# Optimization experiments

Measured on AMD Instinct MI355X. Metric: run time of the kernel, lower is better.

Reference implementation:

```python
import jax, jax.numpy as jnp
import numpy as np

N = 100000   # nodes
F = 32       # input features
E = 1600000  # edges
G = 512      # graphs
EPS = 1e-5   # BatchNorm eps


def setup_inputs() -> dict:
    key = jax.random.key(0)
    ks = jax.random.split(key, 12)
    x = jax.random.normal(ks[0], (N, F), jnp.float32)
    edge_index = jax.random.randint(ks[1], (2, E), 0, N)
    batch = jnp.sort(jax.random.randint(ks[2], (N,), 0, G))

    def glorot(k, i, o):
        return jax.random.normal(k, (i, o), jnp.float32) * (1.0 / np.sqrt(i))

    return {
        "x": x, "edge_index": edge_index, "batch": batch,
        "W1": glorot(ks[3], F, 16), "b1": jnp.zeros((16,), jnp.float32),
        "g1": jnp.ones((16,), jnp.float32), "be1": jnp.zeros((16,), jnp.float32),
        "W2": glorot(ks[4], 16, 64), "b2": jnp.zeros((64,), jnp.float32),
        "g2": jnp.ones((64,), jnp.float32), "be2": jnp.zeros((64,), jnp.float32),
        "W3": glorot(ks[5], 64, 64), "b3": jnp.zeros((64,), jnp.float32),
        "Wc": glorot(ks[6], 64, 1), "bc": jnp.zeros((1,), jnp.float32),
    }


def _gcn_conv(h, src, dst, dis, W, b, n):
    # PyG GCNConv: D^{-1/2}(A+I)D^{-1/2} X W + b (self-loops folded in analytically)
    hw = h @ W                                   # [N, out]
    msg = hw[src] * (dis[src] * dis[dst])[:, None]   # gather + normalize, [E, out]
    agg = jax.ops.segment_sum(msg, dst, num_segments=n)  # scatter-add
    agg = agg + hw * (dis * dis)[:, None]        # self-loop contribution
    return agg + b


def _bn(h, g, b):
    # BatchNorm1d, training mode (biased variance over node axis)
    m = jnp.mean(h, axis=0)
    v = jnp.mean((h - m) ** 2, axis=0)
    return (h - m) * jax.lax.rsqrt(v + EPS) * g + b


def reference(x, edge_index, batch, W1, b1, g1, be1, W2, b2, g2, be2, W3, b3, Wc, bc):
    n = x.shape[0]
    src, dst = edge_index[0], edge_index[1]
    # degree including self-loops (computed on target nodes, edge weight 1)
    deg = jax.ops.segment_sum(jnp.ones((src.shape[0],), x.dtype), dst, num_segments=n) + 1.0
    dis = jax.lax.rsqrt(deg)

    h = jnp.tanh(_gcn_conv(x, src, dst, dis, W1, b1, n))
    h = _bn(h, g1, be1)
    h = jnp.tanh(_gcn_conv(h, src, dst, dis, W2, b2, n))
    h = _bn(h, g2, be2)
    h = jnp.tanh(_gcn_conv(h, src, dst, dis, W3, b3, n))

    # global_mean_pool over graph ids
    sums = jax.ops.segment_sum(h, batch, num_segments=G)          # [G, 64]
    cnts = jax.ops.segment_sum(jnp.ones((n,), x.dtype), batch, num_segments=G)
    pooled = sums / jnp.maximum(cnts, 1.0)[:, None]

    return pooled @ Wc + bc   # [G, 1]
```

## Files before the change

kernel.cpp:

```cpp
#include <hip/hip_runtime.h>

#define EPSV 1e-5f
#define EB 512
#define NPB 256
#define NBUK_MAX 512
#define FCAP 12288

typedef __attribute__((ext_vector_type(8))) short bf16x8;
typedef __attribute__((ext_vector_type(4))) float f32x4;
typedef unsigned short ushort_t;

__device__ inline unsigned f2bf(float f){
  unsigned u = __float_as_uint(f);
  u += 0x7fffu + ((u>>16)&1u);
  return u>>16;
}
#define BF_LO(u) __uint_as_float((u)<<16)
#define BF_HI(u) __uint_as_float((u)&0xffff0000u)

__global__ __launch_bounds__(256) void k_csr_count(const int* __restrict__ dst, int E, int chunk,
                                                   int nbuk, int* __restrict__ cnt){
  __shared__ int hist[NBUK_MAX];
  int t = threadIdx.x, b = blockIdx.x;
  for(int k=t; k<nbuk; k+=256) hist[k]=0;
  __syncthreads();
  int lo = b*chunk, hi = lo+chunk < E ? lo+chunk : E;
  for(int i=lo+t*4; i+3<hi; i+=1024){
    int4 d4 = *(const int4*)(dst + i);
    atomicAdd(&hist[d4.x>>8], 1); atomicAdd(&hist[d4.y>>8], 1);
    atomicAdd(&hist[d4.z>>8], 1); atomicAdd(&hist[d4.w>>8], 1);
  }
  int rem = lo + ((hi - lo) & ~3);
  for(int i=rem+t; i<hi; i+=256) atomicAdd(&hist[dst[i]>>8], 1);
  __syncthreads();
  for(int k=t; k<nbuk; k+=256) cnt[(size_t)k*EB + b] = hist[k];
}

__global__ __launch_bounds__(1024) void k_scan_local(const int* __restrict__ v_in, int L,
                                                     int* __restrict__ loc, int* __restrict__ blk){
  __shared__ int ps[1024];
  int t = threadIdx.x;
  int i = blockIdx.x*1024 + t;
  int v = (i < L) ? v_in[i] : 0;
  ps[t] = v;
  __syncthreads();
  for(int off=1; off<1024; off<<=1){
    int u = (t>=off) ? ps[t-off] : 0;
    __syncthreads();
    ps[t] += u;
    __syncthreads();
  }
  if(i < L) loc[i] = ps[t] - v;
  if(t == 1023) blk[blockIdx.x] = ps[t];
}

__global__ __launch_bounds__(1024) void k_scan_sums(int* __restrict__ blk, int nb,
                                                    int* __restrict__ totalOut){
  __shared__ int ps[1024];
  int t = threadIdx.x;
  int v = (t < nb) ? blk[t] : 0;
  ps[t] = v;
  __syncthreads();
  for(int off=1; off<1024; off<<=1){
    int u = (t>=off) ? ps[t-off] : 0;
    __syncthreads();
    ps[t] += u;
    __syncthreads();
  }
  if(t < nb) blk[t] = ps[t] - v;
  if(t == 1023) *totalOut = ps[t];
}

__global__ __launch_bounds__(256) void k_csr_scatter(const int* __restrict__ src,
                                                     const int* __restrict__ dst,
                                                     const int* __restrict__ loc,
                                                     const int* __restrict__ blk,
                                                     int E, int chunk, int nbuk,
                                                     unsigned* __restrict__ epk){
  __shared__ int cur[NBUK_MAX];
  int t = threadIdx.x, b = blockIdx.x;
  for(int k=t; k<nbuk; k+=256){
    int i = k*EB + b;
    cur[k] = loc[i] + blk[i>>10];
  }
  __syncthreads();
  int lo = b*chunk, hi = lo+chunk < E ? lo+chunk : E;
  for(int i=lo+t*4; i+3<hi; i+=1024){
    int4 s4 = *(const int4*)(src + i);
    int4 d4 = *(const int4*)(dst + i);
    int p0 = atomicAdd(&cur[d4.x>>8], 1);
    epk[p0] = ((unsigned)s4.x<<8) | (unsigned)(d4.x & 255);
    int p1 = atomicAdd(&cur[d4.y>>8], 1);
    epk[p1] = ((unsigned)s4.y<<8) | (unsigned)(d4.y & 255);
    int p2 = atomicAdd(&cur[d4.z>>8], 1);
    epk[p2] = ((unsigned)s4.z<<8) | (unsigned)(d4.z & 255);
    int p3 = atomicAdd(&cur[d4.w>>8], 1);
    epk[p3] = ((unsigned)s4.w<<8) | (unsigned)(d4.w & 255);
  }
  int rem = lo + ((hi - lo) & ~3);
  for(int i=rem+t; i<hi; i+=256){
    int d = dst[i];
    int p = atomicAdd(&cur[d>>8], 1);
    epk[p] = ((unsigned)src[i]<<8) | (unsigned)(d & 255);
  }
}

__global__ __launch_bounds__(256) void k_csr_final(const unsigned* __restrict__ epk,
                                                   const int* __restrict__ loc,
                                                   const int* __restrict__ blk,
                                                   int nbuk, int N, int E,
                                                   int* __restrict__ rp, float* __restrict__ dis,
                                                   int* __restrict__ csr_src){
  __shared__ int hist[NPB], ps[NPB], cur[NPB];
  __shared__ unsigned eld[FCAP];
  int t = threadIdx.x, k = blockIdx.x;
  int i0 = k*EB;
  int base = loc[i0] + blk[i0>>10];
  int next;
  if(k+1 < nbuk){ int i1 = (k+1)*EB; next = loc[i1] + blk[i1>>10]; }
  else next = E;
  int cntk = next - base;
  int node0 = k*NPB;
  bool inLds = (cntk <= FCAP);
  hist[t] = 0;
  __syncthreads();
  if(inLds){
    for(int i=t; i<cntk; i+=256){
      unsigned e = epk[base+i];
      eld[i] = e;
      atomicAdd(&hist[(int)(e & 255u)], 1);
    }
  } else {
    for(int i=t; i<cntk; i+=256) atomicAdd(&hist[(int)(epk[base+i] & 255u)], 1);
  }
  __syncthreads();
  int deg = hist[t];
  ps[t] = deg;
  __syncthreads();
  for(int off=1; off<256; off<<=1){
    int u = (t>=off) ? ps[t-off] : 0;
    __syncthreads();
    ps[t] += u;
    __syncthreads();
  }
  int lb = ps[t] - deg;
  int n = node0 + t;
  if(n < N){
    rp[n]  = base + lb;
    dis[n] = rsqrtf((float)deg + 1.0f);
  }
  cur[t] = base + lb;
  __syncthreads();
  if(inLds){
    for(int i=t; i<cntk; i+=256){
      unsigned e = eld[i];
      int p = atomicAdd(&cur[(int)(e & 255u)], 1);
      csr_src[p] = (int)(e >> 8);
    }
  } else {
    for(int i=t; i<cntk; i+=256){
      unsigned e = epk[base+i];
      int p = atomicAdd(&cur[(int)(e & 255u)], 1);
      csr_src[p] = (int)(e >> 8);
    }
  }
  if(k == nbuk-1 && t == 0) rp[N] = E;
}

__global__ __launch_bounds__(256) void k_gemm1(const float* __restrict__ x,
                                               const float* __restrict__ W,
                                               const float* __restrict__ dis,
                                               int N, ushort_t* __restrict__ P1){
  __shared__ __align__(16) float Ws[32*16];
  int t = threadIdx.x;
  for(int i=t; i<32*16; i+=256) Ws[i] = W[i];
  __syncthreads();
  int row = blockIdx.x*256 + t;
  if(row >= N) return;
  const float4* xr = (const float4*)(x + (size_t)row*32);
  float acc[16];
  #pragma unroll
  for(int j=0;j<16;j++) acc[j]=0.f;
  #pragma unroll
  for(int k4=0;k4<8;k4++){
    float4 v = xr[k4];
    float vv[4] = {v.x, v.y, v.z, v.w};
    #pragma unroll
    for(int kk=0;kk<4;kk++){
      float h = vv[kk];
      const float* wr = &Ws[(k4*4+kk)*16];
      #pragma unroll
      for(int j=0;j<16;j++) acc[j] += h*wr[j];
    }
  }
  float d = dis[row];
  unsigned q[8];
  #pragma unroll
  for(int j=0;j<8;j++)
    q[j] = f2bf(acc[2*j]*d) | (f2bf(acc[2*j+1]*d)<<16);
  uint4* o = (uint4*)(P1 + (size_t)row*16);
  o[0] = make_uint4(q[0],q[1],q[2],q[3]);
  o[1] = make_uint4(q[4],q[5],q[6],q[7]);
}

__global__ __launch_bounds__(256) void k_gather1(const int* __restrict__ rp,
    const int* __restrict__ csr_src,
    const float* __restrict__ dis, const ushort_t* __restrict__ P1,
    const float* __restrict__ bias, int N, ushort_t* __restrict__ Q1,
    float* __restrict__ sdis, float* __restrict__ partials){
  int t = threadIdx.x;
  int idx = blockIdx.x*256 + t;
  int n = idx >> 1, g = t & 1;
  float v[8];
  #pragma unroll
  for(int j=0;j<8;j++) v[j]=0.f;

  if(n < N){
    int beg = rp[n], end = rp[n+1];
    const uint4* Pv = (const uint4*)P1;
    uint4 u = Pv[(size_t)n*2 + g];
    float a0 = BF_LO(u.x), a1 = BF_HI(u.x), a2 = BF_LO(u.y), a3 = BF_HI(u.y);
    float a4 = BF_LO(u.z), a5 = BF_HI(u.z), a6 = BF_LO(u.w), a7 = BF_HI(u.w);
    float b0=0.f,b1=0.f,b2=0.f,b3=0.f,b4=0.f,b5=0.f,b6=0.f,b7=0.f;
    float sd = 0.f;
    int j = beg;
    for(; j+3 < end; j += 4){
      int s0 = csr_src[j], s1 = csr_src[j+1], s2 = csr_src[j+2], s3 = csr_src[j+3];
      uint4 u0 = Pv[(size_t)s0*2 + g];
      uint4 u1 = Pv[(size_t)s1*2 + g];
      uint4 u2 = Pv[(size_t)s2*2 + g];
      uint4 u3 = Pv[(size_t)s3*2 + g];
      if(g==0) sd += (dis[s0] + dis[s1]) + (dis[s2] + dis[s3]);
      a0 += BF_LO(u0.x); a1 += BF_HI(u0.x); a2 += BF_LO(u0.y); a3 += BF_HI(u0.y);
      a4 += BF_LO(u0.z); a5 += BF_HI(u0.z); a6 += BF_LO(u0.w); a7 += BF_HI(u0.w);
      b0 += BF_LO(u1.x); b1 += BF_HI(u1.x); b2 += BF_LO(u1.y); b3 += BF_HI(u1.y);
      b4 += BF_LO(u1.z); b5 += BF_HI(u1.z); b6 += BF_LO(u1.w); b7 += BF_HI(u1.w);
      a0 += BF_LO(u2.x); a1 += BF_HI(u2.x); a2 += BF_LO(u2.y); a3 += BF_HI(u2.y);
      a4 += BF_LO(u2.z); a5 += BF_HI(u2.z); a6 += BF_LO(u2.w); a7 += BF_HI(u2.w);
      b0 += BF_LO(u3.x); b1 += BF_HI(u3.x); b2 += BF_LO(u3.y); b3 += BF_HI(u3.y);
      b4 += BF_LO(u3.z); b5 += BF_HI(u3.z); b6 += BF_LO(u3.w); b7 += BF_HI(u3.w);
    }
    for(; j < end; ++j){
      int s0 = csr_src[j];
      uint4 u0 = Pv[(size_t)s0*2 + g];
      if(g==0) sd += dis[s0];
      a0 += BF_LO(u0.x); a1 += BF_HI(u0.x); a2 += BF_LO(u0.y); a3 += BF_HI(u0.y);
      a4 += BF_LO(u0.z); a5 += BF_HI(u0.z); a6 += BF_LO(u0.w); a7 += BF_HI(u0.w);
    }
    float d = dis[n];
    float4 bb0 = *(const float4*)(bias + g*8);
    float4 bb1 = *(const float4*)(bias + g*8 + 4);
    v[0] = tanhf((a0+b0)*d + bb0.x); v[1] = tanhf((a1+b1)*d + bb0.y);
    v[2] = tanhf((a2+b2)*d + bb0.z); v[3] = tanhf((a3+b3)*d + bb0.w);
    v[4] = tanhf((a4+b4)*d + bb1.x); v[5] = tanhf((a5+b5)*d + bb1.y);
    v[6] = tanhf((a6+b6)*d + bb1.z); v[7] = tanhf((a7+b7)*d + bb1.w);
    uint4 o;
    o.x = f2bf(v[0]*d) | (f2bf(v[1]*d)<<16);
    o.y = f2bf(v[2]*d) | (f2bf(v[3]*d)<<16);
    o.z = f2bf(v[4]*d) | (f2bf(v[5]*d)<<16);
    o.w = f2bf(v[6]*d) | (f2bf(v[7]*d)<<16);
    *(uint4*)(Q1 + (size_t)n*16 + g*8) = o;
    if(g==0) sdis[n] = sd;
  }

  int lane = t & 63, wid = t >> 6;
  __shared__ float redS[4][2][8], redQ[4][2][8];
  #pragma unroll
  for(int j=0;j<8;j++){
    float s = v[j], q = v[j]*v[j];
    #pragma unroll
    for(int off=32; off>=2; off>>=1){
      s += __shfl_down(s, off, 64);
      q += __shfl_down(q, off, 64);
    }
    if(lane < 2){ redS[wid][lane][j] = s; redQ[wid][lane][j] = q; }
  }
  __syncthreads();
  if(t < 16){
    int gg = t>>3, j = t&7;
    float S = redS[0][gg][j]+redS[1][gg][j]+redS[2][gg][j]+redS[3][gg][j];
    float Q = redQ[0][gg][j]+redQ[1][gg][j]+redQ[2][gg][j]+redQ[3][gg][j];
    partials[(size_t)blockIdx.x*32 + t]      = S;
    partials[(size_t)blockIdx.x*32 + 16 + t] = Q;
  }
}

template<int C>
__global__ __launch_bounds__(256) void k_bn_red(const float* __restrict__ partials, int nblk,
                                                float* __restrict__ red){
  constexpr int W = 2*C;
  constexpr int RPF = 256/W;
  int t = threadIdx.x;
  int c = t % W, r0 = t / W;
  float acc = 0.f;
  for(int r = blockIdx.x*RPF + r0; r < nblk; r += 64*RPF)
    acc += partials[(size_t)r*W + c];
  __shared__ float ls[256];
  ls[t] = acc;
  __syncthreads();
  if(t < W){
    float s = 0.f;
    #pragma unroll
    for(int k=0;k<RPF;k++) s += ls[k*W + t];
    red[blockIdx.x*W + t] = s;
  }
}

__global__ __launch_bounds__(256) void k_bn_finprep2b(const float* __restrict__ red,
                           const float* __restrict__ gw, const float* __restrict__ be,
                           float invN, const float* __restrict__ W,
                           ushort_t* __restrict__ wf, float* __restrict__ cp){
  __shared__ float s0[16], s1[16], scf[16], shf[16];
  int t = threadIdx.x;
  if(t < 32){
    float s = 0.f;
    for(int r=0;r<64;r++) s += red[r*32 + t];
    if(t < 16) s0[t] = s; else s1[t-16] = s;
  }
  __syncthreads();
  if(t < 16){
    float m = s0[t]*invN;
    float var = fmaxf(s1[t]*invN - m*m, 0.f);
    float inv = rsqrtf(var + EPSV);
    float sc = gw[t]*inv;
    scf[t] = sc;
    shf[t] = be[t] - m*sc;
  }
  __syncthreads();
  int total = 4*64*8;
  for(int idx=t; idx<total; idx+=256){
    int e = idx & 7;
    int l = (idx>>3) & 63;
    int ct = idx>>9;
    int k = (l>>4)*8 + e;
    int col = ct*16 + (l&15);
    float v = (k < 16) ? scf[k]*W[k*64 + col] : 0.f;
    wf[idx] = (ushort_t)f2bf(v);
  }
  if(t < 64){
    float s = 0.f;
    for(int k=0;k<16;k++) s += shf[k]*W[k*64 + t];
    cp[t] = s;
  }
}

__global__ __launch_bounds__(256) void k_bn_finprep3(const float* __restrict__ red,
                           const float* __restrict__ gw, const float* __restrict__ be,
                           float invN, const float* __restrict__ W,
                           ushort_t* __restrict__ wf, float* __restrict__ cp){
  __shared__ float s0[64], s1[64], scf[64], shf[64];
  int t = threadIdx.x;
  if(t < 128){
    float s = 0.f;
    for(int r=0;r<64;r++) s += red[r*128 + t];
    if(t < 64) s0[t] = s; else s1[t-64] = s;
  }
  __syncthreads();
  if(t < 64){
    float m = s0[t]*invN;
    float var = fmaxf(s1[t]*invN - m*m, 0.f);
    float inv = rsqrtf(var + EPSV);
    float sc = gw[t]*inv;
    scf[t] = sc;
    shf[t] = be[t] - m*sc;
  }
  __syncthreads();
  int total = 4*2*64*8;
  for(int idx=t; idx<total; idx+=256){
    int e = idx & 7;
    int l = (idx>>3) & 63;
    int slot = idx>>9;
    int ct = slot>>1, half = slot&1;
    int k = (l>>4)*8 + e + half*32;
    int col = ct*16 + (l&15);
    wf[idx] = (ushort_t)f2bf(scf[k]*W[k*64 + col]);
  }
  if(t < 64){
    float s = 0.f;
    for(int k=0;k<64;k++) s += shf[k]*W[k*64 + t];
    cp[t] = s;
  }
}

__global__ __launch_bounds__(256) void k_gather2(const int* __restrict__ rp,
    const int* __restrict__ csr_src, const ushort_t* __restrict__ Q1,
    int N, ushort_t* __restrict__ M2){
  int t = threadIdx.x;
  int idx = blockIdx.x*256 + t;
  int n = idx >> 1, g = t & 1;
  if(n >= N) return;
  int beg = rp[n], end = rp[n+1];
  const uint4* Pv = (const uint4*)Q1;
  uint4 u = Pv[(size_t)n*2 + g];
  float a0 = BF_LO(u.x), a1 = BF_HI(u.x), a2 = BF_LO(u.y), a3 = BF_HI(u.y);
  float a4 = BF_LO(u.z), a5 = BF_HI(u.z), a6 = BF_LO(u.w), a7 = BF_HI(u.w);
  float b0=0.f,b1=0.f,b2=0.f,b3=0.f,b4=0.f,b5=0.f,b6=0.f,b7=0.f;
  int j = beg;
  for(; j+3 < end; j += 4){
    int s0 = csr_src[j], s1 = csr_src[j+1], s2 = csr_src[j+2], s3 = csr_src[j+3];
    uint4 u0 = Pv[(size_t)s0*2 + g];
    uint4 u1 = Pv[(size_t)s1*2 + g];
    uint4 u2 = Pv[(size_t)s2*2 + g];
    uint4 u3 = Pv[(size_t)s3*2 + g];
    a0 += BF_LO(u0.x); a1 += BF_HI(u0.x); a2 += BF_LO(u0.y); a3 += BF_HI(u0.y);
    a4 += BF_LO(u0.z); a5 += BF_HI(u0.z); a6 += BF_LO(u0.w); a7 += BF_HI(u0.w);
    b0 += BF_LO(u1.x); b1 += BF_HI(u1.x); b2 += BF_LO(u1.y); b3 += BF_HI(u1.y);
    b4 += BF_LO(u1.z); b5 += BF_HI(u1.z); b6 += BF_LO(u1.w); b7 += BF_HI(u1.w);
    a0 += BF_LO(u2.x); a1 += BF_HI(u2.x); a2 += BF_LO(u2.y); a3 += BF_HI(u2.y);
    a4 += BF_LO(u2.z); a5 += BF_HI(u2.z); a6 += BF_LO(u2.w); a7 += BF_HI(u2.w);
    b0 += BF_LO(u3.x); b1 += BF_HI(u3.x); b2 += BF_LO(u3.y); b3 += BF_HI(u3.y);
    b4 += BF_LO(u3.z); b5 += BF_HI(u3.z); b6 += BF_LO(u3.w); b7 += BF_HI(u3.w);
  }
  for(; j < end; ++j){
    int s0 = csr_src[j];
    uint4 u0 = Pv[(size_t)s0*2 + g];
    a0 += BF_LO(u0.x); a1 += BF_HI(u0.x); a2 += BF_LO(u0.y); a3 += BF_HI(u0.y);
    a4 += BF_LO(u0.z); a5 += BF_HI(u0.z); a6 += BF_LO(u0.w); a7 += BF_HI(u0.w);
  }
  uint4 o;
  o.x = f2bf(a0+b0) | (f2bf(a1+b1)<<16);
  o.y = f2bf(a2+b2) | (f2bf(a3+b3)<<16);
  o.z = f2bf(a4+b4) | (f2bf(a5+b5)<<16);
  o.w = f2bf(a6+b6) | (f2bf(a7+b7)<<16);
  *(uint4*)(M2 + (size_t)n*16 + g*8) = o;
}

__global__ __launch_bounds__(256) void k_mfma2(const ushort_t* __restrict__ M2,
                                               const ushort_t* __restrict__ wf,
                                               const float* __restrict__ cp,
                                               const float* __restrict__ dis,
                                               const float* __restrict__ sdis,
                                               const float* __restrict__ b2,
                                               int N, ushort_t* __restrict__ Q2,
                                               float* __restrict__ partials){
  int t = threadIdx.x, wid = t>>6, l = t&63;
  int r0 = blockIdx.x*128 + wid*32;

  bf16x8 bfr[4];
  #pragma unroll
  for(int ct=0; ct<4; ct++)
    bfr[ct] = *(const bf16x8*)(wf + ((size_t)ct*64 + l)*8);

  bf16x8 af[2];
  #pragma unroll
  for(int rt=0; rt<2; rt++){
    int arow = r0 + rt*16 + (l&15);
    int k0 = (l>>4)*8;
    if(arow < N && k0 < 16) af[rt] = *(const bf16x8*)(M2 + (size_t)arow*16 + k0);
    else                    af[rt] = (bf16x8){0,0,0,0,0,0,0,0};
  }

  f32x4 acc[2][4];
  #pragma unroll
  for(int rt=0; rt<2; rt++)
    #pragma unroll
    for(int ct=0; ct<4; ct++)
      acc[rt][ct] = (f32x4){0.f,0.f,0.f,0.f};

  #pragma unroll
  for(int rt=0; rt<2; rt++)
    #pragma unroll
    for(int ct=0; ct<4; ct++)
      acc[rt][ct] = __builtin_amdgcn_mfma_f32_16x16x32_bf16(af[rt], bfr[ct], acc[rt][ct], 0, 0, 0);

  float cpc[4], blc[4];
  #pragma unroll
  for(int ct=0; ct<4; ct++){
    int col = ct*16 + (l&15);
    cpc[ct] = cp[col]; blc[ct] = b2[col];
  }

  float S4[4] = {0.f,0.f,0.f,0.f}, Q4[4] = {0.f,0.f,0.f,0.f};
  #pragma unroll
  for(int rt=0; rt<2; rt++){
    int rbase = r0 + rt*16 + (l>>4)*4;
    #pragma unroll
    for(int reg=0; reg<4; reg++){
      int row = rbase + reg;
      if(row < N){
        float d = dis[row];
        float sg = sdis[row] + d;
        #pragma unroll
        for(int ct=0; ct<4; ct++){
          float h = tanhf(d*(acc[rt][ct][reg] + sg*cpc[ct]) + blc[ct]);
          Q2[(size_t)row*64 + ct*16 + (l&15)] = (ushort_t)f2bf(h*d);
          S4[ct] += h; Q4[ct] += h*h;
        }
      }
    }
  }
  #pragma unroll
  for(int ct=0; ct<4; ct++){
    S4[ct] += __shfl_xor(S4[ct], 16, 64);
    S4[ct] += __shfl_xor(S4[ct], 32, 64);
    Q4[ct] += __shfl_xor(Q4[ct], 16, 64);
    Q4[ct] += __shfl_xor(Q4[ct], 32, 64);
  }
  __shared__ float wsm[4][64], wqm[4][64];
  if(l < 16){
    #pragma unroll
    for(int ct=0; ct<4; ct++){
      wsm[wid][ct*16 + l] = S4[ct];
      wqm[wid][ct*16 + l] = Q4[ct];
    }
  }
  __syncthreads();
  if(t < 64){
    float S = wsm[0][t]+wsm[1][t]+wsm[2][t]+wsm[3][t];
    float Q = wqm[0][t]+wqm[1][t]+wqm[2][t]+wqm[3][t];
    partials[(size_t)blockIdx.x*128 + t]      = S;
    partials[(size_t)blockIdx.x*128 + 64 + t] = Q;
  }
}

__global__ __launch_bounds__(256) void k_gather3(const int* __restrict__ rp,
    const int* __restrict__ csr_src, const ushort_t* __restrict__ Q2,
    int N, ushort_t* __restrict__ M3){
  int t = threadIdx.x;
  int idx = blockIdx.x*256 + t;
  int n = idx >> 3, g = t & 7;
  if(n >= N) return;
  int beg = rp[n], end = rp[n+1];
  const uint4* Pv = (const uint4*)Q2;
  uint4 u = Pv[(size_t)n*8 + g];
  float a0 = BF_LO(u.x), a1 = BF_HI(u.x), a2 = BF_LO(u.y), a3 = BF_HI(u.y);
  float a4 = BF_LO(u.z), a5 = BF_HI(u.z), a6 = BF_LO(u.w), a7 = BF_HI(u.w);
  float b0=0.f,b1=0.f,b2=0.f,b3=0.f,b4=0.f,b5=0.f,b6=0.f,b7=0.f;
  int j = beg;
  for(; j+3 < end; j += 4){
    int s0 = csr_src[j], s1 = csr_src[j+1], s2 = csr_src[j+2], s3 = csr_src[j+3];
    uint4 u0 = Pv[(size_t)s0*8 + g];
    uint4 u1 = Pv[(size_t)s1*8 + g];
    uint4 u2 = Pv[(size_t)s2*8 + g];
    uint4 u3 = Pv[(size_t)s3*8 + g];
    a0 += BF_LO(u0.x); a1 += BF_HI(u0.x); a2 += BF_LO(u0.y); a3 += BF_HI(u0.y);
    a4 += BF_LO(u0.z); a5 += BF_HI(u0.z); a6 += BF_LO(u0.w); a7 += BF_HI(u0.w);
    b0 += BF_LO(u1.x); b1 += BF_HI(u1.x); b2 += BF_LO(u1.y); b3 += BF_HI(u1.y);
    b4 += BF_LO(u1.z); b5 += BF_HI(u1.z); b6 += BF_LO(u1.w); b7 += BF_HI(u1.w);
    a0 += BF_LO(u2.x); a1 += BF_HI(u2.x); a2 += BF_LO(u2.y); a3 += BF_HI(u2.y);
    a4 += BF_LO(u2.z); a5 += BF_HI(u2.z); a6 += BF_LO(u2.w); a7 += BF_HI(u2.w);
    b0 += BF_LO(u3.x); b1 += BF_HI(u3.x); b2 += BF_LO(u3.y); b3 += BF_HI(u3.y);
    b4 += BF_LO(u3.z); b5 += BF_HI(u3.z); b6 += BF_LO(u3.w); b7 += BF_HI(u3.w);
  }
  for(; j < end; ++j){
    int s0 = csr_src[j];
    uint4 u0 = Pv[(size_t)s0*8 + g];
    a0 += BF_LO(u0.x); a1 += BF_HI(u0.x); a2 += BF_LO(u0.y); a3 += BF_HI(u0.y);
    a4 += BF_LO(u0.z); a5 += BF_HI(u0.z); a6 += BF_LO(u0.w); a7 += BF_HI(u0.w);
  }
  uint4 o;
  o.x = f2bf(a0+b0) | (f2bf(a1+b1)<<16);
  o.y = f2bf(a2+b2) | (f2bf(a3+b3)<<16);
  o.z = f2bf(a4+b4) | (f2bf(a5+b5)<<16);
  o.w = f2bf(a6+b6) | (f2bf(a7+b7)<<16);
  *(uint4*)(M3 + (size_t)n*8*8 + g*8) = o;
}

__global__ __launch_bounds__(256) void k_mfma_head(const ushort_t* __restrict__ M3,
                                                   const ushort_t* __restrict__ wf,
                                                   const float* __restrict__ cp,
                                                   const float* __restrict__ dis,
                                                   const float* __restrict__ sdis,
                                                   const float* __restrict__ b3,
                                                   const float* __restrict__ Wc,
                                                   int N, float* __restrict__ y){
  int t = threadIdx.x, wid = t>>6, l = t&63;
  int r0 = blockIdx.x*128 + wid*32;

  bf16x8 bfr[4][2];
  #pragma unroll
  for(int ct=0; ct<4; ct++)
    #pragma unroll
    for(int h=0; h<2; h++)
      bfr[ct][h] = *(const bf16x8*)(wf + ((size_t)(ct*2+h)*64 + l)*8);

  bf16x8 af[2][2];
  #pragma unroll
  for(int rt=0; rt<2; rt++){
    int arow = r0 + rt*16 + (l&15);
    int k0 = (l>>4)*8;
    #pragma unroll
    for(int h=0; h<2; h++){
      if(arow < N) af[rt][h] = *(const bf16x8*)(M3 + (size_t)arow*64 + k0 + h*32);
      else         af[rt][h] = (bf16x8){0,0,0,0,0,0,0,0};
    }
  }

  f32x4 acc[2][4];
  #pragma unroll
  for(int rt=0; rt<2; rt++)
    #pragma unroll
    for(int ct=0; ct<4; ct++)
      acc[rt][ct] = (f32x4){0.f,0.f,0.f,0.f};

  #pragma unroll
  for(int rt=0; rt<2; rt++)
    #pragma unroll
    for(int ct=0; ct<4; ct++)
      #pragma unroll
      for(int h=0; h<2; h++)
        acc[rt][ct] = __builtin_amdgcn_mfma_f32_16x16x32_bf16(af[rt][h], bfr[ct][h], acc[rt][ct], 0, 0, 0);

  float cpc[4], blc[4], wcc[4];
  #pragma unroll
  for(int ct=0; ct<4; ct++){
    int col = ct*16 + (l&15);
    cpc[ct] = cp[col]; blc[ct] = b3[col]; wcc[ct] = Wc[col];
  }

  #pragma unroll
  for(int rt=0; rt<2; rt++){
    int rbase = r0 + rt*16 + (l>>4)*4;
    #pragma unroll
    for(int reg=0; reg<4; reg++){
      int row = rbase + reg;
      bool ok = (row < N);
      float d  = ok ? dis[row] : 0.f;
      float sg = ok ? (sdis[row] + d) : 0.f;
      float s = 0.f;
      #pragma unroll
      for(int ct=0; ct<4; ct++){
        float h = tanhf(d*(acc[rt][ct][reg] + sg*cpc[ct]) + blc[ct]);
        s += h*wcc[ct];
      }
      s += __shfl_xor(s, 1, 64);
      s += __shfl_xor(s, 2, 64);
      s += __shfl_xor(s, 4, 64);
      s += __shfl_xor(s, 8, 64);
      if(ok && (l&15)==0) y[row] = s;
    }
  }
}

__global__ __launch_bounds__(64) void k_pool2(const float* __restrict__ y,
                                              const int* __restrict__ batch, int N,
                                              const float* __restrict__ bc,
                                              float* __restrict__ out){
  int gId = blockIdx.x;
  int t = threadIdx.x;
  int lo=0, hi=N;
  while(lo<hi){ int mid=(lo+hi)>>1; if(batch[mid] < gId) lo=mid+1; else hi=mid; }
  int start = lo;
  lo=start; hi=N;
  while(lo<hi){ int mid=(lo+hi)>>1; if(batch[mid] < gId+1) lo=mid+1; else hi=mid; }
  int end = lo;

  float s = 0.f;
  for(int r = start+t; r < end; r += 64) s += y[r];
  #pragma unroll
  for(int o=32; o>0; o>>=1) s += __shfl_down(s, o, 64);
  if(t == 0){
    float cnt = (float)(end - start);
    out[gId] = s / fmaxf(cnt, 1.0f) + bc[0];
  }
}

extern "C" void kernel_launch(void* const* d_in, const int* in_sizes, int n_in,
                              void* d_out, int out_size, void* d_ws, size_t ws_size,
                              hipStream_t stream) {
  const float* x     = (const float*)d_in[0];
  const int*   ei    = (const int*)d_in[1];
  const int*   batch = (const int*)d_in[2];
  const float* W1 = (const float*)d_in[3];
  const float* b1 = (const float*)d_in[4];
  const float* g1 = (const float*)d_in[5];
  const float* be1= (const float*)d_in[6];
  const float* W2 = (const float*)d_in[7];
  const float* b2 = (const float*)d_in[8];
  const float* g2 = (const float*)d_in[9];
  const float* be2= (const float*)d_in[10];
  const float* W3 = (const float*)d_in[11];
  const float* b3 = (const float*)d_in[12];
  const float* Wc = (const float*)d_in[13];
  const float* bc = (const float*)d_in[14];

  int N = in_sizes[2];
  int E = in_sizes[1] / 2;
  int G = out_size;
  const int* srcp = ei;
  const int* dstp = ei + E;
  float* out = (float*)d_out;

  auto cdiv = [](long long a, long long b){ return (int)((a+b-1)/b); };
  auto al16 = [](size_t s){ return (s + 15) & ~(size_t)15; };
  int nbuk  = cdiv(N, NPB);
  int chunk = 4*cdiv(E, (long long)EB*4);
  int L     = nbuk * EB;
  int nbL   = cdiv(L, 1024);
  int nblk16 = cdiv((long long)N*2, 256);
  int nblk64 = cdiv((long long)N*8, 256);
  int nblkM  = cdiv(N, 128);

  char* w = (char*)d_ws;
  ushort_t* Q1       = (ushort_t*)w; w += al16((size_t)N*16*2);
  ushort_t* P1       = (ushort_t*)w; w += al16((size_t)N*16*2);
  ushort_t* M2       = (ushort_t*)w; w += al16((size_t)N*16*2);
  ushort_t* Q2       = (ushort_t*)w; w += al16((size_t)N*64*2);
  ushort_t* M3       = (ushort_t*)w; w += al16((size_t)N*64*2);
  float*    dis      = (float*)w;    w += al16((size_t)N*4);
  float*    sdis     = (float*)w;    w += al16((size_t)N*4);
  float*    yv       = (float*)w;    w += al16((size_t)N*4);
  int*      row_ptr  = (int*)w;      w += al16((size_t)(N+1)*4);
  int*      csr_src  = (int*)w;      w += al16((size_t)E*4);
  unsigned* epk      = (unsigned*)w; w += al16((size_t)E*4);
  int*      cnt      = (int*)w;      w += al16((size_t)L*4);
  int*      scan_loc = (int*)w;      w += al16((size_t)L*4);
  int*      scan_blk = (int*)w;      w += al16(1024*4);
  float*    partials = (float*)w;    w += al16((size_t)nblk64*128*4);
  float*    red      = (float*)w;    w += al16(64*128*4);
  float*    cp       = (float*)w;    w += al16(64*4);
  ushort_t* wf       = (ushort_t*)w; w += al16(8*64*8*2);

  k_csr_count<<<EB,256,0,stream>>>(dstp, E, chunk, nbuk, cnt);
  k_scan_local<<<nbL,1024,0,stream>>>(cnt, L, scan_loc, scan_blk);
  k_scan_sums<<<1,1024,0,stream>>>(scan_blk, nbL, row_ptr + N);
  k_csr_scatter<<<EB,256,0,stream>>>(srcp, dstp, scan_loc, scan_blk, E, chunk, nbuk, epk);
  k_csr_final<<<nbuk,256,0,stream>>>(epk, scan_loc, scan_blk, nbuk, N, E, row_ptr, dis, csr_src);

  k_gemm1<<<cdiv(N,256),256,0,stream>>>(x, W1, dis, N, P1);
  k_gather1<<<nblk16,256,0,stream>>>(row_ptr, csr_src, dis, P1, b1, N, Q1, sdis, partials);
  k_bn_red<16><<<64,256,0,stream>>>(partials, nblk16, red);
  k_bn_finprep2b<<<1,256,0,stream>>>(red, g1, be1, 1.0f/N, W2, wf, cp);

  k_gather2<<<nblk16,256,0,stream>>>(row_ptr, csr_src, Q1, N, M2);
  k_mfma2<<<nblkM,256,0,stream>>>(M2, wf, cp, dis, sdis, b2, N, Q2, partials);
  k_bn_red<64><<<64,256,0,stream>>>(partials, nblkM, red);
  k_bn_finprep3<<<1,256,0,stream>>>(red, g2, be2, 1.0f/N, W3, wf, cp);

  k_gather3<<<nblk64,256,0,stream>>>(row_ptr, csr_src, Q2, N, M3);
  k_mfma_head<<<cdiv(N,128),256,0,stream>>>(M3, wf, cp, dis, sdis, b3, Wc, N, yv);

  k_pool2<<<G,64,0,stream>>>(yv, batch, N, bc, out);
}
```

Before: 176.6 us.

## Fuse CSR build and BN reduction stages into cooperative kernels with grid sync

```diff
diff --git a/kernel.cpp b/kernel.cpp
--- a/kernel.cpp
+++ b/kernel.cpp
@@ -1,4 +1,6 @@
 #include <hip/hip_runtime.h>
+#include <hip/hip_cooperative_groups.h>
+namespace cg = cooperative_groups;
 
 #define EPSV 1e-5f
 #define EB 512
@@ -18,153 +20,140 @@
 #define BF_LO(u) __uint_as_float((u)<<16)
 #define BF_HI(u) __uint_as_float((u)&0xffff0000u)
 
-__global__ __launch_bounds__(256) void k_csr_count(const int* __restrict__ dst, int E, int chunk,
-                                                   int nbuk, int* __restrict__ cnt){
-  __shared__ int hist[NBUK_MAX];
+__global__ __launch_bounds__(256) void k_csr_coop(const int* __restrict__ src,
+    const int* __restrict__ dst, int E, int chunk, int nbuk,
+    int* __restrict__ cnt, int* __restrict__ posloc, int* __restrict__ btot,
+    int* __restrict__ bbase, unsigned* __restrict__ epk,
+    int N, int* __restrict__ rp, float* __restrict__ dis, int* __restrict__ csr_src){
+  cg::grid_group grid = cg::this_grid();
+  __shared__ int sA[FCAP];
+  __shared__ int sB[256], sC[256], sD[256];
   int t = threadIdx.x, b = blockIdx.x;
-  for(int k=t; k<nbuk; k+=256) hist[k]=0;
+  int lo = b*chunk, hi = lo+chunk < E ? lo+chunk : E;
+
+  for(int k=t; k<nbuk; k+=256) sA[k]=0;
   __syncthreads();
-  int lo = b*chunk, hi = lo+chunk < E ? lo+chunk : E;
   for(int i=lo+t*4; i+3<hi; i+=1024){
     int4 d4 = *(const int4*)(dst + i);
-    atomicAdd(&hist[d4.x>>8], 1); atomicAdd(&hist[d4.y>>8], 1);
-    atomicAdd(&hist[d4.z>>8], 1); atomicAdd(&hist[d4.w>>8], 1);
-  }
-  int rem = lo + ((hi - lo) & ~3);
-  for(int i=rem+t; i<hi; i+=256) atomicAdd(&hist[dst[i]>>8], 1);
+    atomicAdd(&sA[d4.x>>8],1); atomicAdd(&sA[d4.y>>8],1);
+    atomicAdd(&sA[d4.z>>8],1); atomicAdd(&sA[d4.w>>8],1);
+  }
+  {
+    int rem = lo + ((hi - lo) & ~3);
+    for(int i=rem+t; i<hi; i+=256) atomicAdd(&sA[dst[i]>>8],1);
+  }
   __syncthreads();
-  for(int k=t; k<nbuk; k+=256) cnt[(size_t)k*EB + b] = hist[k];
-}
-
-__global__ __launch_bounds__(1024) void k_scan_local(const int* __restrict__ v_in, int L,
-                                                     int* __restrict__ loc, int* __restrict__ blk){
-  __shared__ int ps[1024];
-  int t = threadIdx.x;
-  int i = blockIdx.x*1024 + t;
-  int v = (i < L) ? v_in[i] : 0;
-  ps[t] = v;
+  for(int k=t; k<nbuk; k+=256) cnt[(size_t)k*EB + b] = sA[k];
+  grid.sync();
+
+  if(b < nbuk){
+    size_t base = (size_t)b*EB;
+    int c0 = cnt[base + 2*t], c1 = cnt[base + 2*t + 1];
+    int s = c0 + c1;
+    sB[t] = s;
+    __syncthreads();
+    for(int off=1; off<256; off<<=1){
+      int u = (t>=off) ? sB[t-off] : 0;
+      __syncthreads();
+      sB[t] += u;
+      __syncthreads();
+    }
+    int ex = sB[t] - s;
+    posloc[base + 2*t]     = ex;
+    posloc[base + 2*t + 1] = ex + c0;
+    if(t == 255) btot[b] = sB[255];
+  }
+  grid.sync();
+
+  if(b == 0){
+    int v0 = (2*t   < nbuk) ? btot[2*t]   : 0;
+    int v1 = (2*t+1 < nbuk) ? btot[2*t+1] : 0;
+    int s = v0 + v1;
+    sB[t] = s;
+    __syncthreads();
+    for(int off=1; off<256; off<<=1){
+      int u = (t>=off) ? sB[t-off] : 0;
+      __syncthreads();
+      sB[t] += u;
+      __syncthreads();
+    }
+    int ex = sB[t] - s;
+    bbase[2*t]   = ex;
+    bbase[2*t+1] = ex + v0;
+    if(t == 0){ bbase[NBUK_MAX] = E; rp[N] = E; }
+  }
+  grid.sync();
+
+  for(int k=t; k<nbuk; k+=256)
+    sA[k] = bbase[k] + posloc[(size_t)k*EB + b];
   __syncthreads();
-  for(int off=1; off<1024; off<<=1){
-    int u = (t>=off) ? ps[t-off] : 0;
-    __syncthreads();
-    ps[t] += u;
-    __syncthreads();
-  }
-  if(i < L) loc[i] = ps[t] - v;
-  if(t == 1023) blk[blockIdx.x] = ps[t];
-}
-
-__global__ __launch_bounds__(1024) void k_scan_sums(int* __restrict__ blk, int nb,
-                                                    int* __restrict__ totalOut){
-  __shared__ int ps[1024];
-  int t = threadIdx.x;
-  int v = (t < nb) ? blk[t] : 0;
-  ps[t] = v;
-  __syncthreads();
-  for(int off=1; off<1024; off<<=1){
-    int u = (t>=off) ? ps[t-off] : 0;
-    __syncthreads();
-    ps[t] += u;
-    __syncthreads();
-  }
-  if(t < nb) blk[t] = ps[t] - v;
-  if(t == 1023) *totalOut = ps[t];
-}
-
-__global__ __launch_bounds__(256) void k_csr_scatter(const int* __restrict__ src,
-                                                     const int* __restrict__ dst,
-                                                     const int* __restrict__ loc,
-                                                     const int* __restrict__ blk,
-                                                     int E, int chunk, int nbuk,
-                                                     unsigned* __restrict__ epk){
-  __shared__ int cur[NBUK_MAX];
-  int t = threadIdx.x, b = blockIdx.x;
-  for(int k=t; k<nbuk; k+=256){
-    int i = k*EB + b;
-    cur[k] = loc[i] + blk[i>>10];
-  }
-  __syncthreads();
-  int lo = b*chunk, hi = lo+chunk < E ? lo+chunk : E;
   for(int i=lo+t*4; i+3<hi; i+=1024){
     int4 s4 = *(const int4*)(src + i);
     int4 d4 = *(const int4*)(dst + i);
-    int p0 = atomicAdd(&cur[d4.x>>8], 1);
-    epk[p0] = ((unsigned)s4.x<<8) | (unsigned)(d4.x & 255);
-    int p1 = atomicAdd(&cur[d4.y>>8], 1);
-    epk[p1] = ((unsigned)s4.y<<8) | (unsigned)(d4.y & 255);
-    int p2 = atomicAdd(&cur[d4.z>>8], 1);
-    epk[p2] = ((unsigned)s4.z<<8) | (unsigned)(d4.z & 255);
-    int p3 = atomicAdd(&cur[d4.w>>8], 1);
-    epk[p3] = ((unsigned)s4.w<<8) | (unsigned)(d4.w & 255);
-  }
-  int rem = lo + ((hi - lo) & ~3);
-  for(int i=rem+t; i<hi; i+=256){
-    int d = dst[i];
-    int p = atomicAdd(&cur[d>>8], 1);
-    epk[p] = ((unsigned)src[i]<<8) | (unsigned)(d & 255);
-  }
-}
-
-__global__ __launch_bounds__(256) void k_csr_final(const unsigned* __restrict__ epk,
-                                                   const int* __restrict__ loc,
-                                                   const int* __restrict__ blk,
-                                                   int nbuk, int N, int E,
-                                                   int* __restrict__ rp, float* __restrict__ dis,
-                                                   int* __restrict__ csr_src){
-  __shared__ int hist[NPB], ps[NPB], cur[NPB];
-  __shared__ unsigned eld[FCAP];
-  int t = threadIdx.x, k = blockIdx.x;
-  int i0 = k*EB;
-  int base = loc[i0] + blk[i0>>10];
-  int next;
-  if(k+1 < nbuk){ int i1 = (k+1)*EB; next = loc[i1] + blk[i1>>10]; }
-  else next = E;
-  int cntk = next - base;
-  int node0 = k*NPB;
-  bool inLds = (cntk <= FCAP);
-  hist[t] = 0;
-  __syncthreads();
-  if(inLds){
-    for(int i=t; i<cntk; i+=256){
-      unsigned e = epk[base+i];
-      eld[i] = e;
-      atomicAdd(&hist[(int)(e & 255u)], 1);
-    }
-  } else {
-    for(int i=t; i<cntk; i+=256) atomicAdd(&hist[(int)(epk[base+i] & 255u)], 1);
-  }
-  __syncthreads();
-  int deg = hist[t];
-  ps[t] = deg;
-  __syncthreads();
-  for(int off=1; off<256; off<<=1){
-    int u = (t>=off) ? ps[t-off] : 0;
-    __syncthreads();
-    ps[t] += u;
-    __syncthreads();
-  }
-  int lb = ps[t] - deg;
-  int n = node0 + t;
-  if(n < N){
-    rp[n]  = base + lb;
-    dis[n] = rsqrtf((float)deg + 1.0f);
-  }
-  cur[t] = base + lb;
-  __syncthreads();
-  if(inLds){
-    for(int i=t; i<cntk; i+=256){
-      unsigned e = eld[i];
-      int p = atomicAdd(&cur[(int)(e & 255u)], 1);
-      csr_src[p] = (int)(e >> 8);
-    }
-  } else {
-    for(int i=t; i<cntk; i+=256){
-      unsigned e = epk[base+i];
-      int p = atomicAdd(&cur[(int)(e & 255u)], 1);
-      csr_src[p] = (int)(e >> 8);
-    }
-  }
-  if(k == nbuk-1 && t == 0) rp[N] = E;
+    int p0 = atomicAdd(&sA[d4.x>>8],1); epk[p0] = ((unsigned)s4.x<<8)|(unsigned)(d4.x&255);
+    int p1 = atomicAdd(&sA[d4.y>>8],1); epk[p1] = ((unsigned)s4.y<<8)|(unsigned)(d4.y&255);
+    int p2 = atomicAdd(&sA[d4.z>>8],1); epk[p2] = ((unsigned)s4.z<<8)|(unsigned)(d4.z&255);
+    int p3 = atomicAdd(&sA[d4.w>>8],1); epk[p3] = ((unsigned)s4.w<<8)|(unsigned)(d4.w&255);
+  }
+  {
+    int rem = lo + ((hi - lo) & ~3);
+    for(int i=rem+t; i<hi; i+=256){
+      int d = dst[i];
+      int p = atomicAdd(&sA[d>>8],1);
+      epk[p] = ((unsigned)src[i]<<8)|(unsigned)(d&255);
+    }
+  }
+  grid.sync();
+
+  if(b < nbuk){
+    int base = bbase[b];
+    int next = bbase[b+1];
+    int cntk = next - base;
+    int node0 = b*NPB;
+    bool inLds = (cntk <= FCAP);
+    sB[t] = 0;
+    __syncthreads();
+    if(inLds){
+      for(int i=t; i<cntk; i+=256){
+        unsigned e = epk[base+i];
+        sA[i] = (int)e;
+        atomicAdd(&sB[(int)(e & 255u)], 1);
+      }
+    } else {
+      for(int i=t; i<cntk; i+=256) atomicAdd(&sB[(int)(epk[base+i] & 255u)], 1);
+    }
+    __syncthreads();
+    int deg = sB[t];
+    sC[t] = deg;
+    __syncthreads();
+    for(int off=1; off<256; off<<=1){
+      int u = (t>=off) ? sC[t-off] : 0;
+      __syncthreads();
+      sC[t] += u;
+      __syncthreads();
+    }
+    int lb = sC[t] - deg;
+    int n = node0 + t;
+    if(n < N){
+      rp[n]  = base + lb;
+      dis[n] = rsqrtf((float)deg + 1.0f);
+    }
+    sD[t] = base + lb;
+    __syncthreads();
+    if(inLds){
+      for(int i=t; i<cntk; i+=256){
+        unsigned e = (unsigned)sA[i];
+        int p = atomicAdd(&sD[(int)(e & 255u)], 1);
+        csr_src[p] = (int)(e >> 8);
+      }
+    } else {
+      for(int i=t; i<cntk; i+=256){
+        unsigned e = epk[base+i];
+        int p = atomicAdd(&sD[(int)(e & 255u)], 1);
+        csr_src[p] = (int)(e >> 8);
+      }
+    }
+  }
 }
 
 __global__ __launch_bounds__(256) void k_gemm1(const float* __restrict__ x,
@@ -285,100 +274,121 @@
   }
 }
 
-template<int C>
-__global__ __launch_bounds__(256) void k_bn_red(const float* __restrict__ partials, int nblk,
-                                                float* __restrict__ red){
-  constexpr int W = 2*C;
-  constexpr int RPF = 256/W;
-  int t = threadIdx.x;
-  int c = t % W, r0 = t / W;
-  float acc = 0.f;
-  for(int r = blockIdx.x*RPF + r0; r < nblk; r += 64*RPF)
-    acc += partials[(size_t)r*W + c];
-  __shared__ float ls[256];
-  ls[t] = acc;
-  __syncthreads();
-  if(t < W){
-    float s = 0.f;
-    #pragma unroll
-    for(int k=0;k<RPF;k++) s += ls[k*W + t];
-    red[blockIdx.x*W + t] = s;
-  }
-}
-
-__global__ __launch_bounds__(256) void k_bn_finprep2b(const float* __restrict__ red,
+__global__ __launch_bounds__(256) void k_bn16_coop(const float* __restrict__ partials, int nblk,
+                           float* __restrict__ red,
                            const float* __restrict__ gw, const float* __restrict__ be,
                            float invN, const float* __restrict__ W,
                            ushort_t* __restrict__ wf, float* __restrict__ cp){
+  cg::grid_group grid = cg::this_grid();
+  __shared__ float ls[256];
   __shared__ float s0[16], s1[16], scf[16], shf[16];
   int t = threadIdx.x;
-  if(t < 32){
-    float s = 0.f;
-    for(int r=0;r<64;r++) s += red[r*32 + t];
-    if(t < 16) s0[t] = s; else s1[t-16] = s;
-  }
-  __syncthreads();
-  if(t < 16){
-    float m = s0[t]*invN;
-    float var = fmaxf(s1[t]*invN - m*m, 0.f);
-    float inv = rsqrtf(var + EPSV);
-    float sc = gw[t]*inv;
-    scf[t] = sc;
-    shf[t] = be[t] - m*sc;
-  }
-  __syncthreads();
-  int total = 4*64*8;
-  for(int idx=t; idx<total; idx+=256){
-    int e = idx & 7;
-    int l = (idx>>3) & 63;
-    int ct = idx>>9;
-    int k = (l>>4)*8 + e;
-    int col = ct*16 + (l&15);
-    float v = (k < 16) ? scf[k]*W[k*64 + col] : 0.f;
-    wf[idx] = (ushort_t)f2bf(v);
-  }
-  if(t < 64){
-    float s = 0.f;
-    for(int k=0;k<16;k++) s += shf[k]*W[k*64 + t];
-    cp[t] = s;
-  }
-}
-
-__global__ __launch_bounds__(256) void k_bn_finprep3(const float* __restrict__ red,
+  {
+    const int Wd = 32, RPF = 8;
+    int c = t % Wd, r0 = t / Wd;
+    float acc = 0.f;
+    for(int r = blockIdx.x*RPF + r0; r < nblk; r += 64*RPF)
+      acc += partials[(size_t)r*Wd + c];
+    ls[t] = acc;
+    __syncthreads();
+    if(t < Wd){
+      float s = 0.f;
+      #pragma unroll
+      for(int k=0;k<RPF;k++) s += ls[k*Wd + t];
+      red[blockIdx.x*Wd + t] = s;
+    }
+  }
+  grid.sync();
+  if(blockIdx.x == 0){
+    if(t < 32){
+      float s = 0.f;
+      for(int r=0;r<64;r++) s += red[r*32 + t];
+      if(t < 16) s0[t] = s; else s1[t-16] = s;
+    }
+    __syncthreads();
+    if(t < 16){
+      float m = s0[t]*invN;
+      float var = fmaxf(s1[t]*invN - m*m, 0.f);
+      float inv = rsqrtf(var + EPSV);
+      float sc = gw[t]*inv;
+      scf[t] = sc;
+      shf[t] = be[t] - m*sc;
+    }
+    __syncthreads();
+    int total = 4*64*8;
+    for(int idx=t; idx<total; idx+=256){
+      int e = idx & 7;
+      int l = (idx>>3) & 63;
+      int ct = idx>>9;
+      int k = (l>>4)*8 + e;
+      int col = ct*16 + (l&15);
+      float v = (k < 16) ? scf[k]*W[k*64 + col] : 0.f;
+      wf[idx] = (ushort_t)f2bf(v);
+    }
+    if(t < 64){
+      float s = 0.f;
+      for(int k=0;k<16;k++) s += shf[k]*W[k*64 + t];
+      cp[t] = s;
+    }
+  }
+}
+
+__global__ __launch_bounds__(256) void k_bn64_coop(const float* __restrict__ partials, int nblk,
+                           float* __restrict__ red,
                            const float* __restrict__ gw, const float* __restrict__ be,
                            float invN, const float* __restrict__ W,
                            ushort_t* __restrict__ wf, float* __restrict__ cp){
+  cg::grid_group grid = cg::this_grid();
+  __shared__ float ls[256];
   __shared__ float s0[64], s1[64], scf[64], shf[64];
   int t = threadIdx.x;
-  if(t < 128){
-    float s = 0.f;
-    for(int r=0;r<64;r++) s += red[r*128 + t];
-    if(t < 64) s0[t] = s; else s1[t-64] = s;
-  }
-  __syncthreads();
-  if(t < 64){
-    float m = s0[t]*invN;
-    float var = fmaxf(s1[t]*invN - m*m, 0.f);
-    float inv = rsqrtf(var + EPSV);
-    float sc = gw[t]*inv;
-    scf[t] = sc;
-    shf[t] = be[t] - m*sc;
-  }
-  __syncthreads();
-  int total = 4*2*64*8;
-  for(int idx=t; idx<total; idx+=256){
-    int e = idx & 7;
-    int l = (idx>>3) & 63;
-    int slot = idx>>9;
-    int ct = slot>>1, half = slot&1;
-    int k = (l>>4)*8 + e + half*32;
-    int col = ct*16 + (l&15);
-    wf[idx] = (ushort_t)f2bf(scf[k]*W[k*64 + col]);
-  }
-  if(t < 64){
-    float s = 0.f;
-    for(int k=0;k<64;k++) s += shf[k]*W[k*64 + t];
-    cp[t] = s;
+  {
+    const int Wd = 128, RPF = 2;
+    int c = t % Wd, r0 = t / Wd;
+    float acc = 0.f;
+    for(int r = blockIdx.x*RPF + r0; r < nblk; r += 64*RPF)
+      acc += partials[(size_t)r*Wd + c];
+    ls[t] = acc;
+    __syncthreads();
+    if(t < Wd){
+      float s = 0.f;
+      #pragma unroll
+      for(int k=0;k<RPF;k++) s += ls[k*Wd + t];
+      red[blockIdx.x*Wd + t] = s;
+    }
+  }
+  grid.sync();
+  if(blockIdx.x == 0){
+    if(t < 128){
+      float s = 0.f;
+      for(int r=0;r<64;r++) s += red[r*128 + t];
+      if(t < 64) s0[t] = s; else s1[t-64] = s;
+    }
+    __syncthreads();
+    if(t < 64){
+      float m = s0[t]*invN;
+      float var = fmaxf(s1[t]*invN - m*m, 0.f);
+      float inv = rsqrtf(var + EPSV);
+      float sc = gw[t]*inv;
+      scf[t] = sc;
+      shf[t] = be[t] - m*sc;
+    }
+    __syncthreads();
+    int total = 4*2*64*8;
+    for(int idx=t; idx<total; idx+=256){
+      int e = idx & 7;
+      int l = (idx>>3) & 63;
+      int slot = idx>>9;
+      int ct = slot>>1, half = slot&1;
+      int k = (l>>4)*8 + e + half*32;
+      int col = ct*16 + (l&15);
+      wf[idx] = (ushort_t)f2bf(scf[k]*W[k*64 + col]);
+    }
+    if(t < 64){
+      float s = 0.f;
+      for(int k=0;k<64;k++) s += shf[k]*W[k*64 + t];
+      cp[t] = s;
+    }
   }
 }
 
@@ -686,7 +696,6 @@
   int nbuk  = cdiv(N, NPB);
   int chunk = 4*cdiv(E, (long long)EB*4);
   int L     = nbuk * EB;
-  int nbL   = cdiv(L, 1024);
   int nblk16 = cdiv((long long)N*2, 256);
   int nblk64 = cdiv((long long)N*8, 256);
   int nblkM  = cdiv(N, 128);
@@ -704,28 +713,38 @@
   int*      csr_src  = (int*)w;      w += al16((size_t)E*4);
   unsigned* epk      = (unsigned*)w; w += al16((size_t)E*4);
   int*      cnt      = (int*)w;      w += al16((size_t)L*4);
-  int*      scan_loc = (int*)w;      w += al16((size_t)L*4);
-  int*      scan_blk = (int*)w;      w += al16(1024*4);
+  int*      posloc   = (int*)w;      w += al16((size_t)L*4);
+  int*      btot     = (int*)w;      w += al16((size_t)NBUK_MAX*4);
+  int*      bbase    = (int*)w;      w += al16((size_t)(NBUK_MAX+1)*4);
   float*    partials = (float*)w;    w += al16((size_t)nblk64*128*4);
   float*    red      = (float*)w;    w += al16(64*128*4);
   float*    cp       = (float*)w;    w += al16(64*4);
   ushort_t* wf       = (ushort_t*)w; w += al16(8*64*8*2);
 
-  k_csr_count<<<EB,256,0,stream>>>(dstp, E, chunk, nbuk, cnt);
-  k_scan_local<<<nbL,1024,0,stream>>>(cnt, L, scan_loc, scan_blk);
-  k_scan_sums<<<1,1024,0,stream>>>(scan_blk, nbL, row_ptr + N);
-  k_csr_scatter<<<EB,256,0,stream>>>(srcp, dstp, scan_loc, scan_blk, E, chunk, nbuk, epk);
-  k_csr_final<<<nbuk,256,0,stream>>>(epk, scan_loc, scan_blk, nbuk, N, E, row_ptr, dis, csr_src);
+  {
+    void* args[] = { (void*)&srcp, (void*)&dstp, (void*)&E, (void*)&chunk, (void*)&nbuk,
+                     (void*)&cnt, (void*)&posloc, (void*)&btot, (void*)&bbase, (void*)&epk,
+                     (void*)&N, (void*)&row_ptr, (void*)&dis, (void*)&csr_src };
+    hipLaunchCooperativeKernel((const void*)k_csr_coop, dim3(EB), dim3(256), args, 0, stream);
+  }
 
   k_gemm1<<<cdiv(N,256),256,0,stream>>>(x, W1, dis, N, P1);
   k_gather1<<<nblk16,256,0,stream>>>(row_ptr, csr_src, dis, P1, b1, N, Q1, sdis, partials);
-  k_bn_red<16><<<64,256,0,stream>>>(partials, nblk16, red);
-  k_bn_finprep2b<<<1,256,0,stream>>>(red, g1, be1, 1.0f/N, W2, wf, cp);
+  {
+    float invN = 1.0f/N;
+    void* args[] = { (void*)&partials, (void*)&nblk16, (void*)&red, (void*)&g1, (void*)&be1,
+                     (void*)&invN, (void*)&W2, (void*)&wf, (void*)&cp };
+    hipLaunchCooperativeKernel((const void*)k_bn16_coop, dim3(64), dim3(256), args, 0, stream);
+  }
 
   k_gather2<<<nblk16,256,0,stream>>>(row_ptr, csr_src, Q1, N, M2);
   k_mfma2<<<nblkM,256,0,stream>>>(M2, wf, cp, dis, sdis, b2, N, Q2, partials);
-  k_bn_red<64><<<64,256,0,stream>>>(partials, nblkM, red);
-  k_bn_finprep3<<<1,256,0,stream>>>(red, g2, be2, 1.0f/N, W3, wf, cp);
+  {
+    float invN = 1.0f/N;
+    void* args[] = { (void*)&partials, (void*)&nblkM, (void*)&red, (void*)&g2, (void*)&be2,
+                     (void*)&invN, (void*)&W3, (void*)&wf, (void*)&cp };
+    hipLaunchCooperativeKernel((const void*)k_bn64_coop, dim3(64), dim3(256), args, 0, stream);
+  }
 
   k_gather3<<<nblk64,256,0,stream>>>(row_ptr, csr_src, Q2, N, M3);
   k_mfma_head<<<cdiv(N,128),256,0,stream>>>(M3, wf, cp, dis, sdis, b3, Wc, N, yv);
```

New measurement: 461.6 us. 2.61x slower.
